# Performance work log

Hardware: AMD Instinct MI355X
Metric: run time of the kernel (lower is better)

## Reference

```python
import jax, jax.numpy as jnp
import numpy as np

T, D = 4096, 1536          # tokens, hidden
H, KV, HD = 24, 8, 64      # heads, kv heads, head dim
E, TOPK, F = 32, 8, 512    # experts, top-k, expert intermediate
FS = 1024                  # shared-MLP intermediate
THETA = 10000.0
AMULT = 0.015625           # attention_multiplier (replaces 1/sqrt(hd))
RMULT = 0.22               # residual_multiplier
EPS = 1e-6


def setup_inputs() -> dict:
    key = jax.random.key(0)
    ks = jax.random.split(key, 12)
    s = 0.02
    return {
        'positions': jnp.arange(T, dtype=jnp.int32),
        'hidden_states': jax.random.normal(ks[0], (T, D), jnp.float32),
        'ln1_w': jnp.ones((D,), jnp.float32),
        'wq': jax.random.normal(ks[1], (D, H * HD), jnp.float32) * s,
        'wk': jax.random.normal(ks[2], (D, KV * HD), jnp.float32) * s,
        'wv': jax.random.normal(ks[3], (D, KV * HD), jnp.float32) * s,
        'wo': jax.random.normal(ks[4], (H * HD, D), jnp.float32) * s,
        'ln2_w': jnp.ones((D,), jnp.float32),
        'router_w': jax.random.normal(ks[5], (D, E), jnp.float32) * s,
        'w_gate_up': jax.random.normal(ks[6], (E, D, 2 * F), jnp.float32) * s,
        'w_down': jax.random.normal(ks[7], (E, F, D), jnp.float32) * s,
        'shared_gate_up': jax.random.normal(ks[8], (D, 2 * FS), jnp.float32) * s,
        'shared_down': jax.random.normal(ks[9], (FS, D), jnp.float32) * s,
    }


def _rmsnorm(x, w):
    var = jnp.mean(x * x, axis=-1, keepdims=True)
    return x * jax.lax.rsqrt(var + EPS) * w


def _rope(x, positions):
    # x: [T, nH, HD], neox-style half rotation
    half = HD // 2
    inv_freq = 1.0 / (THETA ** (jnp.arange(half, dtype=jnp.float32) / half))
    ang = positions.astype(jnp.float32)[:, None] * inv_freq[None, :]  # [T, half]
    cos, sin = jnp.cos(ang)[:, None, :], jnp.sin(ang)[:, None, :]
    x1, x2 = x[..., :half], x[..., half:]
    return jnp.concatenate([x1 * cos - x2 * sin, x2 * cos + x1 * sin], axis=-1)


def _silu_and_mul(gu):
    g, u = jnp.split(gu, 2, axis=-1)
    return jax.nn.silu(g) * u


def reference(positions, hidden_states, ln1_w, wq, wk, wv, wo, ln2_w,
              router_w, w_gate_up, w_down, shared_gate_up, shared_down):
    # ---- attention block ----
    residual = hidden_states
    h = _rmsnorm(hidden_states, ln1_w)
    q = _rope((h @ wq).reshape(T, H, HD), positions)
    k = _rope((h @ wk).reshape(T, KV, HD), positions)
    v = (h @ wv).reshape(T, KV, HD)
    k = jnp.repeat(k, H // KV, axis=1)  # GQA expand -> [T, H, HD]
    v = jnp.repeat(v, H // KV, axis=1)
    scores = jnp.einsum('thd,shd->hts', q, k) * AMULT
    mask = jnp.tril(jnp.ones((T, T), dtype=bool))
    scores = jnp.where(mask[None], scores, jnp.finfo(scores.dtype).min)
    probs = jax.nn.softmax(scores, axis=-1)
    attn = jnp.einsum('hts,shd->thd', probs, v).reshape(T, H * HD) @ wo
    hidden = residual + attn * RMULT

    # ---- MoE + shared MLP block ----
    residual = hidden
    h = _rmsnorm(hidden, ln2_w)
    # router: top-k logits, softmax over selected (renormalized gates)
    logits = h @ router_w                          # [T, E]
    topv, topi = jax.lax.top_k(logits, TOPK)       # [T, TOPK]
    gates = jax.nn.softmax(topv, axis=-1)
    # per-token dense expert weight map [T, E] (zero for unselected experts)
    wmap = jnp.sum(jax.nn.one_hot(topi, E, dtype=h.dtype) * gates[..., None], axis=1)
    gu = jnp.einsum('td,edf->tef', h, w_gate_up)   # [T, E, 2F]
    act = _silu_and_mul(gu)                        # [T, E, F]
    moe_out = jnp.einsum('tef,efd,te->td', act, w_down, wmap)
    # shared SiLU MLP
    shared = _silu_and_mul(h @ shared_gate_up) @ shared_down
    hidden = residual + (moe_out + shared) * RMULT
    return hidden
```

## Files before the change

kernel.cpp:

```cpp
#include <hip/hip_runtime.h>
#include <stdint.h>

using u16 = unsigned short;
using u32 = unsigned int;

typedef __attribute__((ext_vector_type(8))) short short8;
typedef __attribute__((ext_vector_type(4))) short short4v;
typedef __attribute__((ext_vector_type(4))) float f32x4;

#define MFMA16(a,b,c) __builtin_amdgcn_mfma_f32_16x16x32_bf16(a,b,c,0,0,0)
#define QSCL 0.022542110325192448f


__device__ __forceinline__ u16 f2bf(float f){
  u32 u = __float_as_uint(f);
  u += 0x7fffu + ((u>>16)&1u);
  return (u16)(u>>16);
}
__device__ __forceinline__ float bf2f(u16 b){ return __uint_as_float(((u32)b)<<16); }

__device__ __forceinline__ void gload16(const void* g, void* l){
  __builtin_amdgcn_global_load_lds(
      (const __attribute__((address_space(1))) u32*)g,
      (__attribute__((address_space(3))) u32*)l, 16, 0, 0);
}

template<int CTRL>
__device__ __forceinline__ float dppf(float x){
  return __int_as_float(__builtin_amdgcn_mov_dpp(__float_as_int(x), CTRL, 0xf, 0xf, true));
}
__device__ __forceinline__ float red16_sum(float x){
  x += dppf<0x128>(x);
  x += dppf<0x124>(x);
  x += dppf<0x122>(x);
  x += dppf<0x121>(x);
  return x;
}

__global__ __launch_bounds__(256) void k_wt(const float* __restrict__ src,
    u16* __restrict__ dst, int K, int N, long sstride, long dstride)
{
  __shared__ float tile[64][65];
  int nb = blockIdx.x*64, kb = blockIdx.y*64;
  const float* S = src + (long)blockIdx.z*sstride;
  u16* D = dst + (long)blockIdx.z*dstride;
  int tid = threadIdx.x;
  int rr = tid>>4, c4 = (tid&15)*4;
  #pragma unroll
  for (int p=0;p<4;++p){
    int r = p*16 + rr;
    f32x4 v = *(const f32x4*)&S[(long)(kb+r)*N + nb + c4];
    tile[r][c4+0]=v[0]; tile[r][c4+1]=v[1]; tile[r][c4+2]=v[2]; tile[r][c4+3]=v[3];
  }
  __syncthreads();
  #pragma unroll
  for (int p=0;p<4;++p){
    int nn = p*16 + rr;
    short4v o;
    #pragma unroll
    for (int i=0;i<4;++i) o[i] = (short)f2bf(tile[c4+i][nn]);
    *(short4v*)&D[(long)(nb+nn)*K + kb + c4] = o;
  }
}

__global__ __launch_bounds__(256) void k_wti(const float* __restrict__ src,
    u16* __restrict__ dst, int K, int N, int halfN, long sstride, long dstride)
{
  __shared__ float tile[64][65];
  int nb = blockIdx.x*64, kb = blockIdx.y*64;
  const float* S = src + (long)blockIdx.z*sstride;
  u16* D = dst + (long)blockIdx.z*dstride;
  int tid = threadIdx.x;
  int rr = tid>>4, c4 = (tid&15)*4;
  int scol = (nb>>1) + ((c4>>5)<<4) + (c4&15) + (((c4>>4)&1)? halfN : 0);
  #pragma unroll
  for (int p=0;p<4;++p){
    int r = p*16 + rr;
    f32x4 v = *(const f32x4*)&S[(long)(kb+r)*N + scol];
    tile[r][c4+0]=v[0]; tile[r][c4+1]=v[1]; tile[r][c4+2]=v[2]; tile[r][c4+3]=v[3];
  }
  __syncthreads();
  #pragma unroll
  for (int p=0;p<4;++p){
    int nn = p*16 + rr;
    short4v o;
    #pragma unroll
    for (int i=0;i<4;++i) o[i] = (short)f2bf(tile[c4+i][nn]);
    *(short4v*)&D[(long)(nb+nn)*K + kb + c4] = o;
  }
}

__global__ __launch_bounds__(256) void k_vt(const u16* __restrict__ v,
                                            u16* __restrict__ vT)
{
  __shared__ u16 t_[64*72];
  int t0 = blockIdx.x*64, kvh = blockIdx.y;
  int tid = threadIdx.x;
  #pragma unroll
  for (int i=0;i<2;++i){
    int c = tid + i*256;
    int row = c>>3, dc = (c&7)*8;
    *(short8*)&t_[row*72 + dc] = *(const short8*)&v[(long)(t0+row)*2560 + kvh*64 + dc];
  }
  __syncthreads();
  #pragma unroll
  for (int i=0;i<2;++i){
    int c = tid + i*256;
    int d = c>>3, tc = (c&7)*8;
    short8 o;
    #pragma unroll
    for (int j=0;j<8;++j) o[j] = (short)t_[(tc+j)*72 + d];
    *(short8*)&vT[(long)(kvh*64 + d)*4096 + t0 + tc] = o;
  }
}

__global__ __launch_bounds__(192) void k_rmsnorm(const float* __restrict__ x,
                                                 const float* __restrict__ w,
                                                 u16* __restrict__ o)
{
  int t = blockIdx.x, tid = threadIdx.x;
  const float* xr = x + (size_t)t*1536 + tid*8;
  f32x4 a = *(const f32x4*)xr;
  f32x4 b = *(const f32x4*)(xr+4);
  float ss = a[0]*a[0]+a[1]*a[1]+a[2]*a[2]+a[3]*a[3]
           + b[0]*b[0]+b[1]*b[1]+b[2]*b[2]+b[3]*b[3];
  #pragma unroll
  for (int m=1;m<64;m<<=1) ss += __shfl_xor(ss,m);
  __shared__ float red[3];
  if ((tid&63)==0) red[tid>>6]=ss;
  __syncthreads();
  float inv = rsqrtf((red[0]+red[1]+red[2])*(1.0f/1536.0f)+1e-6f);
  const float* wp = w + tid*8;
  f32x4 wa = *(const f32x4*)wp;
  f32x4 wb = *(const f32x4*)(wp+4);
  u16* op = o + (size_t)t*1536 + tid*8;
  #pragma unroll
  for (int j=0;j<4;++j) op[j]   = f2bf(a[j]*inv*wa[j]);
  #pragma unroll
  for (int j=0;j<4;++j) op[j+4] = f2bf(b[j]*inv*wb[j]);
}

template<int MODE, int GATHER>
__global__ __launch_bounds__(256, (MODE==5||MODE==6)?4:3) void k_gemm(
    const u16* __restrict__ A, int lda,
    const u16* __restrict__ Bt, long strideB, int K,
    int Mfix, const int* __restrict__ cnts, const int* __restrict__ offs,
    const int* __restrict__ toks, const float* __restrict__ gates,
    u16* __restrict__ Cb, int ldcb,
    float* __restrict__ Cf, int ldcf,
    const float* __restrict__ resid, const int* __restrict__ pos)
{
  int e = blockIdx.z;
  int M = cnts ? cnts[e] : Mfix;
  int m0 = blockIdx.y*128;
  if (m0 >= M) return;
  int roff = offs ? offs[e] : 0;
  const u16* Bp = Bt + (long)e*strideB;
  int col0 = blockIdx.x*128;

  __shared__ u16 Ash[4096];
  __shared__ u16 Bsh[4096];

  int tid = threadIdx.x, wv = tid>>6, lane = tid&63;
  int lr = lane&15, lg = lane>>4;
  int wr = (wv>>1)*64, wc = (wv&1)*64;

  int row0 = tid>>2, kc = (tid&3)*8;
  int gr0 = min(m0 + row0,      M-1);
  int gr1 = min(m0 + row0 + 64, M-1);
  int ar0, ar1;
  if (GATHER){ ar0 = toks[roff + gr0]; ar1 = toks[roff + gr1]; }
  else       { ar0 = roff + gr0;       ar1 = roff + gr1; }
  const u16* ap0 = A + (long)ar0*lda + kc;
  const u16* ap1 = A + (long)ar1*lda + kc;
  const u16* bp0 = Bp + (long)(col0 + row0)*K + kc;
  const u16* bp1 = bp0 + (long)64*K;

  u16* As0 = &Ash[wv*512];  u16* As1 = &Ash[2048 + wv*512];
  u16* Bs0 = &Bsh[wv*512];  u16* Bs1 = &Bsh[2048 + wv*512];

  f32x4 acc[4][4];
  #pragma unroll
  for (int m=0;m<4;++m)
    #pragma unroll
    for (int n=0;n<4;++n)
      acc[m][n] = (f32x4){0.f,0.f,0.f,0.f};

  int nk = K>>5;
  for (int kt=0; kt<nk; ++kt){
    __syncthreads();
    gload16(ap0, As0); gload16(ap1, As1);
    gload16(bp0, Bs0); gload16(bp1, Bs1);
    ap0 += 32; ap1 += 32; bp0 += 32; bp1 += 32;
    __syncthreads();

    short8 af[4], b1[4];
    #pragma unroll
    for (int m=0;m<4;++m) af[m] = *(const short8*)&Ash[(wr+m*16+lr)*32 + lg*8];
    #pragma unroll
    for (int n=0;n<4;++n) b1[n] = *(const short8*)&Bsh[(wc+n*16+lr)*32 + lg*8];
    #pragma unroll
    for (int m=0;m<4;++m)
      #pragma unroll
      for (int n=0;n<4;++n)
        acc[m][n] = MFMA16(af[m], b1[n], acc[m][n]);
  }

  if constexpr(MODE==6){
    #pragma unroll
    for (int m=0;m<4;++m)
      #pragma unroll
      for (int np=0;np<2;++np)
        #pragma unroll
        for (int rr=0;rr<4;++rr){
          int row = wr + m*16 + lg*4 + rr;
          int gr = m0 + row;
          if (gr >= M) continue;
          float g = acc[m][2*np][rr];
          float u = acc[m][2*np+1][rr];
          float s = g/(1.f+__expf(-g))*u;
          int j = (wc>>1) + np*16 + lr;
          Cb[(long)(roff+gr)*ldcb + (col0>>1) + j] = f2bf(s);
        }
  } else if constexpr(MODE==7){
    if (col0 < 2048){
      float invf0 = __expf(-(float)lr      * 0.28782313662425574f);
      float invf1 = __expf(-(float)(lr+16) * 0.28782313662425574f);
      float qs = (col0 < 1536) ? QSCL : 1.0f;
      #pragma unroll
      for (int m=0;m<4;++m)
        #pragma unroll
        for (int rr=0;rr<4;++rr){
          int gr = m0 + wr + m*16 + lg*4 + rr;
          float pv = (float)pos[gr];
          #pragma unroll
          for (int n=0;n<2;++n){
            float sn, cs;
            __sincosf(pv * (n ? invf1 : invf0), &sn, &cs);
            float x1 = acc[m][n][rr], x2 = acc[m][n+2][rr];
            long base = (long)gr*ldcb + col0 + wc + n*16 + lr;
            Cb[base]      = f2bf((x1*cs - x2*sn)*qs);
            Cb[base + 32] = f2bf((x2*cs + x1*sn)*qs);
          }
        }
    } else {
      #pragma unroll
      for (int m=0;m<4;++m)
        #pragma unroll
        for (int n=0;n<4;++n)
          #pragma unroll
          for (int rr=0;rr<4;++rr){
            int gr = m0 + wr + m*16 + lg*4 + rr;
            int col = wc + n*16 + lr;
            Cb[(long)gr*ldcb + col0 + col] = f2bf(acc[m][n][rr]);
          }
    }
  } else {
    #pragma unroll
    for (int m=0;m<4;++m)
      #pragma unroll
      for (int n=0;n<4;++n)
        #pragma unroll
        for (int rr=0;rr<4;++rr){
          int row = wr + m*16 + lg*4 + rr;
          int gr = m0 + row;
          if (gr >= M) continue;
          int col = wc + n*16 + lr;
          float va = acc[m][n][rr];
          if constexpr(MODE==0){
            Cb[(long)(roff+gr)*ldcb + col0 + col] = f2bf(va);
          } else if constexpr(MODE==1){
            long idx = (long)gr*ldcf + col0 + col;
            Cf[idx] = resid[idx] + va*0.22f;
          } else if constexpr(MODE==5){
            float gt = gates[roff+gr];
            Cb[(long)(roff+gr)*ldcb + col0 + col] = f2bf(va*gt);
          }
        }
  }
}

__global__ __launch_bounds__(192) void k_moesum(const u16* __restrict__ part,
    const int* __restrict__ inv, float* __restrict__ out)
{
  int t = blockIdx.x, tid = threadIdx.x;
  int c = tid*8;
  float s[8] = {0.f,0.f,0.f,0.f,0.f,0.f,0.f,0.f};
  #pragma unroll
  for (int kk=0;kk<8;++kk){
    int slot = inv[t*8+kk];
    short8 v = *(const short8*)&part[(long)slot*1536 + c];
    #pragma unroll
    for (int j=0;j<8;++j) s[j] += bf2f((u16)v[j]);
  }
  float* op = out + (long)t*1536 + c;
  f32x4 o0 = *(const f32x4*)op;
  f32x4 o1 = *(const f32x4*)(op+4);
  #pragma unroll
  for (int j=0;j<4;++j){ o0[j] += s[j]; o1[j] += s[j+4]; }
  *(f32x4*)op = o0;
  *(f32x4*)(op+4) = o1;
}

__global__ __launch_bounds__(256,3) void k_attn(const u16* __restrict__ qg,
    const u16* __restrict__ kg, const u16* __restrict__ vT,
    u16* __restrict__ og, u16* __restrict__ Opart, float* __restrict__ mlb)
{
  int bid = blockIdx.x;
  int kvh = bid & 7;
  int ii = bid >> 3;
  int qt, kt0, kt1, chunk; bool single;
  if (ii < 32)      { qt = 32+ii;        chunk = 0; kt0 = 0;  kt1 = 32;   single = false; }
  else if (ii < 64) { qt = ii;           chunk = 1; kt0 = 32; kt1 = qt+1; single = false; }
  else              { qt = 31-(ii-64);   chunk = 0; kt0 = 0;  kt1 = qt+1; single = true;  }

  int tid = threadIdx.x, wv = tid>>6, lane = tid&63;
  int lr = lane&15, lg = lane>>4;
  __shared__ u16 Ksh[64*72];
  __shared__ u16 Vsh[64*72];
  __shared__ u16 Psh[4][16*72];
  int q0 = qt*64;
  int qrow = q0 + wv*16 + lr;
  short8 qf[3][2];
  #pragma unroll
  for (int hh=0;hh<3;++hh)
    #pragma unroll
    for (int c=0;c<2;++c)
      qf[hh][c] = *(const short8*)&qg[(long)qrow*2560 + (kvh*3+hh)*64 + c*32 + lg*8];

  float l_[3][4];
  f32x4 Ot[3][4];
  #pragma unroll
  for (int hh=0;hh<3;++hh)
    #pragma unroll
    for (int r=0;r<4;++r) l_[hh][r]=0.f;
  #pragma unroll
  for (int hh=0;hh<3;++hh)
    #pragma unroll
    for (int d=0;d<4;++d) Ot[hh][d]=(f32x4){0.f,0.f,0.f,0.f};

  int srow = tid>>3, sdc = (tid&7)*8;
  short8 kreg[2], vreg[2];
  auto loadKV = [&](int kt){
    #pragma unroll
    for (int i=0;i<2;++i){
      int row = srow + i*32;
      kreg[i] = *(const short8*)&kg[(long)(kt*64+row)*2560 + kvh*64 + sdc];
      vreg[i] = *(const short8*)&vT[(long)(kvh*64 + row)*4096 + kt*64 + sdc];
    }
  };
  loadKV(kt0);

  for (int kt=kt0; kt<kt1; ++kt){
    __syncthreads();
    #pragma unroll
    for (int i=0;i<2;++i){
      int row = srow + i*32;
      *(short8*)&Ksh[row*72 + sdc] = kreg[i];
      *(short8*)&Vsh[row*72 + sdc] = vreg[i];
    }
    __syncthreads();
    if (kt < kt1-1) loadKV(kt+1);
    bool diag = (kt==qt);

    #pragma unroll
    for (int hh=0;hh<3;++hh){
      f32x4 S[4];
      #pragma unroll
      for (int n=0;n<4;++n) S[n]=(f32x4){0.f,0.f,0.f,0.f};
      #pragma unroll
      for (int n=0;n<4;++n)
        #pragma unroll
        for (int c=0;c<2;++c){
          short8 kf = *(const short8*)&Ksh[(n*16+lr)*72 + c*32 + lg*8];
          S[n] = MFMA16(qf[hh][c], kf, S[n]);
        }

      float rsum[4] = {0.f,0.f,0.f,0.f};
      #pragma unroll
      for (int n=0;n<4;++n)
        #pragma unroll
        for (int r=0;r<4;++r){
          float sv = S[n][r];
          if (diag){
            int colg = n*16 + lr;
            int rowg = wv*16 + lg*4 + r;
            if (colg > rowg) sv = -1e30f;
          }
          float pv = exp2f(sv);
          S[n][r] = pv;
          rsum[r] += pv;
        }
      #pragma unroll
      for (int r=0;r<4;++r) rsum[r] = red16_sum(rsum[r]);
      #pragma unroll
      for (int r=0;r<4;++r) l_[hh][r] += rsum[r];

      #pragma unroll
      for (int n=0;n<4;++n)
        #pragma unroll
        for (int r=0;r<4;++r)
          Psh[wv][(lg*4+r)*72 + n*16 + lr] = f2bf(S[n][r]);
      #pragma unroll
      for (int c=0;c<2;++c){
        short8 pf = *(const short8*)&Psh[wv][lr*72 + c*32 + lg*8];
        #pragma unroll
        for (int d=0;d<4;++d){
          short8 vf = *(const short8*)&Vsh[(d*16+lr)*72 + c*32 + lg*8];
          Ot[hh][d] = MFMA16(pf, vf, Ot[hh][d]);
        }
      }
    }
  }

  if (single){
    #pragma unroll
    for (int hh=0;hh<3;++hh)
      #pragma unroll
      for (int d=0;d<4;++d)
        #pragma unroll
        for (int r=0;r<4;++r){
          int t = q0 + wv*16 + lg*4 + r;
          og[(long)t*1536 + (kvh*3+hh)*64 + d*16 + lr] = f2bf(Ot[hh][d][r]/l_[hh][r]);
        }
  } else {
    #pragma unroll
    for (int hh=0;hh<3;++hh){
      int h = kvh*3+hh;
      #pragma unroll
      for (int r=0;r<4;++r){
        int t = q0 + wv*16 + lg*4 + r;
        long slot = ((long)(t-2048)*24 + h)*2 + chunk;
        #pragma unroll
        for (int d=0;d<4;++d)
          Opart[slot*64 + d*16 + lr] = f2bf(Ot[hh][d][r]);
        if (lr==0) mlb[slot] = l_[hh][r];
      }
    }
  }
}

__global__ __launch_bounds__(256) void k_comb(const u16* __restrict__ Opart,
    const float* __restrict__ mlb, u16* __restrict__ og)
{
  int gid = blockIdx.x*256 + threadIdx.x;
  int d = gid & 63;
  long rowi = gid >> 6;
  long s0 = rowi*2, s1 = s0+1;
  float l0 = mlb[s0], l1 = mlb[s1];
  float o = (bf2f(Opart[s0*64+d]) + bf2f(Opart[s1*64+d])) / (l0 + l1);
  int t = 2048 + (int)(rowi/24), h = (int)(rowi - (rowi/24)*24);
  og[(long)t*1536 + h*64 + d] = f2bf(o);
}

__global__ __launch_bounds__(256) void k_router(const u16* __restrict__ h2,
    const float* __restrict__ rw, int* __restrict__ topi, float* __restrict__ gatev)
{
  int t = blockIdx.x, tid = threadIdx.x;
  int e = tid & 31, seg = tid >> 5;
  const u16* hr = h2 + (size_t)t*1536 + seg*192;
  const float* wp = rw + (long)seg*192*32 + e;
  float s = 0.f;
  #pragma unroll 4
  for (int d=0; d<192; ++d)
    s += bf2f(hr[d]) * wp[(long)d*32];
  __shared__ float red[8][32];
  red[seg][e] = s;
  __syncthreads();
  __shared__ float lgt[32];
  if (tid < 32){
    float a = 0.f;
    #pragma unroll
    for (int g=0; g<8; ++g) a += red[g][tid];
    lgt[tid] = a;
  }
  __syncthreads();
  if (tid==0){
    u32 msk=0; float tv[8]; int ti[8];
    for (int kk=0;kk<8;++kk){
      float best=-1e30f; int bi=0;
      for (int j2=0;j2<32;++j2)
        if (!((msk>>j2)&1u) && lgt[j2] > best){ best=lgt[j2]; bi=j2; }
      msk |= 1u<<bi; tv[kk]=best; ti[kk]=bi;
    }
    float mx = tv[0], ssum = 0.f, ge[8];
    for (int kk=0;kk<8;++kk){ ge[kk]=__expf(tv[kk]-mx); ssum+=ge[kk]; }
    float isum = 1.f/ssum;
    for (int kk=0;kk<8;++kk){ topi[t*8+kk]=ti[kk]; gatev[t*8+kk]=ge[kk]*isum; }
  }
}

__global__ void k_hist(const int* __restrict__ topi, int* __restrict__ cnt){
  int i = blockIdx.x*256 + threadIdx.x;
  if (i < 4096*8) atomicAdd(&cnt[topi[i]], 1);
}
__global__ void k_scan(const int* __restrict__ cnt, int* __restrict__ offs, int* __restrict__ cur){
  if (threadIdx.x==0 && blockIdx.x==0){
    int a=0;
    for (int e2=0;e2<32;++e2){ offs[e2]=a; cur[e2]=a; a+=cnt[e2]; }
  }
}
__global__ void k_scatter(const int* __restrict__ topi, const float* __restrict__ gatev,
    int* __restrict__ cur, int* __restrict__ toks, float* __restrict__ gts,
    int* __restrict__ inv){
  int i = blockIdx.x*256 + threadIdx.x;
  if (i < 4096*8){
    int e2 = topi[i];
    int p = atomicAdd(&cur[e2], 1);
    toks[p] = i>>3;
    gts[p] = gatev[i]*0.22f;
    inv[i] = p;
  }
}

extern "C" void kernel_launch(void* const* d_in, const int* in_sizes, int n_in,
                              void* d_out, int out_size, void* d_ws, size_t ws_size,
                              hipStream_t stream)
{
  const int*   positions = (const int*)  d_in[0];
  const float* hs   = (const float*)d_in[1];
  const float* ln1w = (const float*)d_in[2];
  const float* wq   = (const float*)d_in[3];
  const float* wk   = (const float*)d_in[4];
  const float* wv   = (const float*)d_in[5];
  const float* wo   = (const float*)d_in[6];
  const float* ln2w = (const float*)d_in[7];
  const float* rww  = (const float*)d_in[8];
  const float* wgu  = (const float*)d_in[9];
  const float* wdn  = (const float*)d_in[10];
  const float* sgu  = (const float*)d_in[11];
  const float* sdn  = (const float*)d_in[12];
  float* out = (float*)d_out;

  char* ws = (char*)d_ws;
  size_t off = 0;
  auto alloc = [&](size_t b)->void*{ void* p = ws + off; off += (b + 255) & ~(size_t)255; return p; };

  u16* hbf     = (u16*)alloc((size_t)4096*1536*2);
  u16* qkv     = (u16*)alloc((size_t)33554432);
  u16* qkvb = qkv;
  u16* aout = qkv + (size_t)4096*2560;
  u16* act_moe = qkv;
  u16* act_sh  = (u16*)alloc((size_t)4096*1024*2);
  u16* vT      = (u16*)alloc((size_t)8*64*4096*2);
  int*   topi  = (int*)  alloc(4096*8*4);
  float* gatev = (float*)alloc(4096*8*4);
  int*   toks  = (int*)  alloc(4096*8*4);
  float* gts   = (float*)alloc(4096*8*4);
  int*   inv   = (int*)  alloc(4096*8*4);
  int*   cnt   = (int*)  alloc(512);
  int*   offs  = (int*)  alloc(512);
  int*   cur   = (int*)  alloc(512);
  u16* wqkvT = (u16*)alloc((size_t)2560*1536*2);
  u16* woT  = (u16*)alloc((size_t)1536*1536*2);
  u16* sguT = (u16*)alloc((size_t)2048*1536*2);
  u16* sdnT = (u16*)alloc((size_t)1536*1024*2);
  u16* wguT = (u16*)alloc((size_t)32*1024*1536*2);
  u16* wdnT = (u16*)alloc((size_t)32*1536*512*2);
  float* hidden2 = out;
  u16*   h2bf = hbf;
  u16*   Opart = hbf;
  float* mlb   = (float*)act_sh;
  u16*   part  = wguT;

  k_wt <<<dim3(24,24,1), 256,0,stream>>>(wq,  wqkvT,                   1536,1536, 0,0);
  k_wt <<<dim3(8,24,1),  256,0,stream>>>(wk,  wqkvT+(size_t)1536*1536, 1536,512,  0,0);
  k_wt <<<dim3(8,24,1),  256,0,stream>>>(wv,  wqkvT+(size_t)2048*1536, 1536,512,  0,0);
  k_wt <<<dim3(24,24,1), 256,0,stream>>>(wo,  woT,  1536,1536, 0,0);
  k_wti<<<dim3(32,24,1), 256,0,stream>>>(sgu, sguT, 1536,2048,1024, 0,0);
  k_wt <<<dim3(24,16,1), 256,0,stream>>>(sdn, sdnT, 1024,1536, 0,0);
  k_wti<<<dim3(16,24,32),256,0,stream>>>(wgu, wguT, 1536,1024,512, (long)1536*1024, (long)1536*1024);
  k_wt <<<dim3(24,8,32), 256,0,stream>>>(wdn, wdnT, 512,1536,  (long)512*1536,  (long)512*1536);

  k_rmsnorm<<<4096,192,0,stream>>>(hs, ln1w, hbf);
  k_gemm<7,0><<<dim3(20,32,1),256,0,stream>>>(hbf,1536, wqkvT,0,1536, 4096,nullptr,nullptr,nullptr,nullptr, qkvb,2560, nullptr,0, nullptr, positions);
  k_vt<<<dim3(64,8,1),256,0,stream>>>(qkvb + 2048, vT);
  k_attn<<<dim3(768,1,1),256,0,stream>>>(qkvb, qkvb + 1536, vT, aout, Opart, mlb);
  k_comb<<<12288,256,0,stream>>>(Opart, mlb, aout);
  k_gemm<1,0><<<dim3(12,32,1),256,0,stream>>>(aout,1536, woT,0,1536, 4096,nullptr,nullptr,nullptr,nullptr, nullptr,0, hidden2,1536, hs, nullptr);
  k_rmsnorm<<<4096,192,0,stream>>>(hidden2, ln2w, h2bf);
  k_router<<<4096,256,0,stream>>>(h2bf, rww, topi, gatev);
  hipMemsetAsync(cnt, 0, 32*4, stream);
  k_hist<<<128,256,0,stream>>>(topi, cnt);
  k_scan<<<1,64,0,stream>>>(cnt, offs, cur);
  k_scatter<<<128,256,0,stream>>>(topi, gatev, cur, toks, gts, inv);
  k_gemm<6,1><<<dim3(8,32,32),256,0,stream>>>(h2bf,1536, wguT,(long)1024*1536,1536, 0,cnt,offs,toks,nullptr, act_moe,512, nullptr,0, nullptr, nullptr);
  k_gemm<6,0><<<dim3(16,32,1),256,0,stream>>>(h2bf,1536, sguT,0,1536, 4096,nullptr,nullptr,nullptr,nullptr, act_sh,1024, nullptr,0, nullptr, nullptr);
  k_gemm<1,0><<<dim3(12,32,1),256,0,stream>>>(act_sh,1024, sdnT,0,1024, 4096,nullptr,nullptr,nullptr,nullptr, nullptr,0, out,1536, out, nullptr);
  k_gemm<5,0><<<dim3(12,32,32),256,0,stream>>>(act_moe,512, wdnT,(long)1536*512,512, 0,cnt,offs,nullptr,gts, part,1536, nullptr,0, nullptr, nullptr);
  k_moesum<<<4096,192,0,stream>>>(part, inv, out);

  (void)in_sizes; (void)n_in; (void)out_size; (void)ws_size;
}
```

Measured before the change: 944.1 us.

## Deepen GEMM K-tile to 64 with XOR-swizzled LDS layout

Doubles the K depth per shared-memory stage from 32 to 64, so each 128x128 tile step performs two MFMA sub-steps per pair of barriers, halving barrier and loop overhead. The global-to-LDS loads are reorganized into four row passes per operand, and the K-chunk index is XOR-swizzled by row so fragment reads from the wider 64-element rows avoid LDS bank conflicts. This doubles LDS use per block (32 KB), which may reduce how many blocks fit per CU under the given launch bounds.

```diff
diff --git a/kernel.cpp b/kernel.cpp
--- a/kernel.cpp
+++ b/kernel.cpp
@@ -158,26 +158,25 @@
   const u16* Bp = Bt + (long)e*strideB;
   int col0 = blockIdx.x*128;
 
-  __shared__ u16 Ash[4096];
-  __shared__ u16 Bsh[4096];
+  __shared__ u16 Ash[128*64];
+  __shared__ u16 Bsh[128*64];
 
   int tid = threadIdx.x, wv = tid>>6, lane = tid&63;
   int lr = lane&15, lg = lane>>4;
   int wr = (wv>>1)*64, wc = (wv&1)*64;
 
-  int row0 = tid>>2, kc = (tid&3)*8;
-  int gr0 = min(m0 + row0,      M-1);
-  int gr1 = min(m0 + row0 + 64, M-1);
-  int ar0, ar1;
-  if (GATHER){ ar0 = toks[roff + gr0]; ar1 = toks[roff + gr1]; }
-  else       { ar0 = roff + gr0;       ar1 = roff + gr1; }
-  const u16* ap0 = A + (long)ar0*lda + kc;
-  const u16* ap1 = A + (long)ar1*lda + kc;
-  const u16* bp0 = Bp + (long)(col0 + row0)*K + kc;
-  const u16* bp1 = bp0 + (long)64*K;
-
-  u16* As0 = &Ash[wv*512];  u16* As1 = &Ash[2048 + wv*512];
-  u16* Bs0 = &Bsh[wv*512];  u16* Bs1 = &Bsh[2048 + wv*512];
+  int rsub = lane>>3;
+  int ksw = ((lane&7) ^ rsub)*8;
+  const u16* apt[4];
+  const u16* bpt[4];
+  #pragma unroll
+  for (int p=0;p<4;++p){
+    int rloc = p*32 + wv*8 + rsub;
+    int gr = min(m0 + rloc, M-1);
+    int ar = GATHER ? toks[roff + gr] : (roff + gr);
+    apt[p] = A + (long)ar*lda + ksw;
+    bpt[p] = Bp + (long)(col0 + rloc)*K + ksw;
+  }
 
   f32x4 acc[4][4];
   #pragma unroll
@@ -186,24 +185,32 @@
     for (int n=0;n<4;++n)
       acc[m][n] = (f32x4){0.f,0.f,0.f,0.f};
 
-  int nk = K>>5;
+  int nk = K>>6;
   for (int kt=0; kt<nk; ++kt){
     __syncthreads();
-    gload16(ap0, As0); gload16(ap1, As1);
-    gload16(bp0, Bs0); gload16(bp1, Bs1);
-    ap0 += 32; ap1 += 32; bp0 += 32; bp1 += 32;
+    #pragma unroll
+    for (int p=0;p<4;++p){
+      gload16(apt[p], &Ash[(p*32 + wv*8)*64]);
+      gload16(bpt[p], &Bsh[(p*32 + wv*8)*64]);
+      apt[p] += 64; bpt[p] += 64;
+    }
     __syncthreads();
 
-    short8 af[4], b1[4];
-    #pragma unroll
-    for (int m=0;m<4;++m) af[m] = *(const short8*)&Ash[(wr+m*16+lr)*32 + lg*8];
-    #pragma unroll
-    for (int n=0;n<4;++n) b1[n] = *(const short8*)&Bsh[(wc+n*16+lr)*32 + lg*8];
-    #pragma unroll
-    for (int m=0;m<4;++m)
+    #pragma unroll
+    for (int kk=0;kk<2;++kk){
+      short8 af[4], b1[4];
+      #pragma unroll
+      for (int m=0;m<4;++m)
+        af[m] = *(const short8*)&Ash[(wr+m*16+lr)*64 + (((kk*4+lg)^(lr&7))*8)];
       #pragma unroll
       for (int n=0;n<4;++n)
-        acc[m][n] = MFMA16(af[m], b1[n], acc[m][n]);
+        b1[n] = *(const short8*)&Bsh[(wc+n*16+lr)*64 + (((kk*4+lg)^(lr&7))*8)];
+      #pragma unroll
+      for (int m=0;m<4;++m)
+        #pragma unroll
+        for (int n=0;n<4;++n)
+          acc[m][n] = MFMA16(af[m], b1[n], acc[m][n]);
+    }
   }
 
   if constexpr(MODE==6){
```

Measured after the change: 893.2 us. 5.4% less time.
